# Kernel tuning notes

Measured on AMD Instinct MI355X. Metric: run time of the kernel, lower is better.

## Reference

```python
import jax, jax.numpy as jnp
import numpy as np
from jax import lax

K = 3          # kernel size
PAD = 1        # padding
STRIDE = 1     # stride (output spatial == input spatial)


def conv2d(x, w, b, pad):
    y = lax.conv_general_dilated(x, w, (1, 1), [(pad, pad), (pad, pad)],
                                 dimension_numbers=("NCHW", "OIHW", "NCHW"))
    return y + b[None, :, None, None]


def bilinear_sample(img, y, x):
    """img: [B,C,H,W]; y,x: [B,Ho,Wo] float coords. Zero outside borders (torchvision semantics)."""
    B, C, H, W = img.shape
    flat = img.reshape(B, C, H * W)
    y0 = jnp.floor(y)
    x0 = jnp.floor(x)
    dy = y - y0
    dx = x - x0

    def gather(yc, xc):
        valid = (yc >= 0) & (yc <= H - 1) & (xc >= 0) & (xc <= W - 1)
        yi = jnp.clip(yc, 0, H - 1).astype(jnp.int32)
        xi = jnp.clip(xc, 0, W - 1).astype(jnp.int32)
        idx = (yi * W + xi).reshape(B, -1)                      # [B, Ho*Wo]
        g = jax.vmap(lambda f, i: f[:, i])(flat, idx)            # [B, C, Ho*Wo]
        g = g.reshape(B, C, y.shape[1], y.shape[2])
        return g * valid[:, None, :, :].astype(img.dtype)

    w00 = ((1 - dy) * (1 - dx))[:, None]
    w01 = ((1 - dy) * dx)[:, None]
    w10 = (dy * (1 - dx))[:, None]
    w11 = (dy * dx)[:, None]
    return (gather(y0, x0) * w00 + gather(y0, x0 + 1) * w01 +
            gather(y0 + 1, x0) * w10 + gather(y0 + 1, x0 + 1) * w11)


def deform_conv2d(feat, offset, weight, bias):
    """feat: [B,C,H,W]; offset: [B,2*K*K,Ho,Wo]; weight: [O,C,K,K]; bias: [O]."""
    B, C, H, W = feat.shape
    Ho, Wo = offset.shape[2], offset.shape[3]
    hh = jnp.arange(Ho, dtype=feat.dtype) * STRIDE - PAD   # base y of kernel origin
    ww = jnp.arange(Wo, dtype=feat.dtype) * STRIDE - PAD
    out = jnp.zeros((B, weight.shape[0], Ho, Wo), feat.dtype)
    for i in range(K):
        for j in range(K):
            k = i * K + j
            sy = hh[None, :, None] + i + offset[:, 2 * k]        # [B,Ho,Wo]
            sx = ww[None, None, :] + j + offset[:, 2 * k + 1]
            sampled = bilinear_sample(feat, sy, sx)               # [B,C,Ho,Wo]
            out = out + jnp.einsum("bchw,oc->bohw", sampled, weight[:, :, i, j])
    return out + bias[None, :, None, None]


def setup_inputs() -> dict:
    key = jax.random.key(0)
    ks = jax.random.split(key, 8)
    IN_CH, OUT_CH = 3, 64
    B, H, W = 4, 256, 256
    s1 = 1.0 / np.sqrt(IN_CH * K * K)
    s2 = 1.0 / np.sqrt(OUT_CH * K * K)
    return {
        "x": jax.random.normal(ks[0], (B, IN_CH, H, W), jnp.float32),
        "conv_w": jax.random.normal(ks[1], (OUT_CH, IN_CH, K, K), jnp.float32) * s1,
        "conv_b": jax.random.normal(ks[2], (OUT_CH,), jnp.float32) * s1,
        "offset_w": jax.random.normal(ks[3], (2 * K * K, OUT_CH, K, K), jnp.float32) * 0.01,
        "offset_b": jax.random.normal(ks[4], (2 * K * K,), jnp.float32) * 0.01,
        "deform_w": jax.random.normal(ks[5], (OUT_CH, OUT_CH, K, K), jnp.float32) * s2,
        "deform_b": jax.random.normal(ks[6], (OUT_CH,), jnp.float32) * s2,
    }


def reference(x, conv_w, conv_b, offset_w, offset_b, deform_w, deform_b):
    feat = conv2d(x, conv_w, conv_b, pad=1)                    # [B,64,H,W]
    offset = conv2d(feat, offset_w, offset_b, pad=PAD)          # [B,18,H,W]
    return deform_conv2d(feat, offset, deform_w, deform_b)
```

## Files before the change

### kernel.cpp

```cpp
#include <hip/hip_runtime.h>
#include <hip/hip_fp16.h>

#define FEAT_N (4*64*256*256)
#define OFFS_N (4*18*256*256)
#define WTF_N  (576*64)
#define WT2F_N (576*32)
#define WT1F_N (4*64*8)

typedef __attribute__((ext_vector_type(8))) _Float16 half8;
typedef __attribute__((ext_vector_type(4))) float float4v;
typedef __attribute__((ext_vector_type(4))) unsigned uint4v;

__device__ __forceinline__ unsigned short f2h(float f) {
    union { __half h; unsigned short u; } c; c.h = __float2half_rn(f); return c.u;
}
__device__ __forceinline__ __half2 u2h2(unsigned u) {
    union { unsigned u; __half2 h; } c; c.u = u; return c.h;
}
__device__ __forceinline__ unsigned h22u(__half2 h) {
    union { __half2 h; unsigned u; } c; c.h = h; return c.u;
}

__global__ __launch_bounds__(256) void prep_weights(const float* __restrict__ dw,
                                                    const float* __restrict__ ow,
                                                    const float* __restrict__ cw,
                                                    unsigned short* __restrict__ wtf,
                                                    unsigned short* __restrict__ wt2f,
                                                    unsigned short* __restrict__ wt1f) {
    int idx = blockIdx.x * 256 + threadIdx.x;
    if (idx < WTF_N) {
        int j    = idx & 7;
        int lane = (idx >> 3) & 63;
        int nt   = (idx >> 9) & 3;
        int ks   = idx >> 11;
        int k    = ks * 32 + ((lane >> 4) << 3) + j;
        int tap  = k >> 6;
        int ic   = k & 63;
        int n    = nt * 16 + (lane & 15);
        wtf[idx] = f2h(dw[n * 576 + ic * 9 + tap]);
    }
    int i2 = idx - WTF_N;
    if (i2 >= 0 && i2 < WT2F_N) {
        int j    = i2 & 7;
        int lane = (i2 >> 3) & 63;
        int nt   = (i2 >> 9) & 1;
        int ks   = i2 >> 10;
        int k    = ks * 32 + ((lane >> 4) << 3) + j;
        int tap  = k >> 6;
        int ic   = k & 63;
        int n    = nt * 16 + (lane & 15);
        wt2f[i2] = (n < 18) ? f2h(ow[n * 576 + ic * 9 + tap]) : (unsigned short)0;
    }
    int i3 = idx - WTF_N - WT2F_N;
    if (i3 >= 0 && i3 < WT1F_N) {
        int j    = i3 & 7;
        int lane = (i3 >> 3) & 63;
        int nt   = (i3 >> 9) & 3;
        int n    = nt * 16 + (lane & 15);
        int k    = ((lane >> 4) << 3) + j;
        wt1f[i3] = (k < 27) ? f2h(cw[n * 27 + k]) : (unsigned short)0;
    }
}

__global__ __launch_bounds__(256) void conv1_kernel(const float* __restrict__ x,
                                                    const unsigned short* __restrict__ wt1f,
                                                    const float* __restrict__ cb,
                                                    unsigned short* __restrict__ featp) {
    __shared__ unsigned short xs[10 * 264];
    const int tid  = threadIdx.x;
    const int lane = tid & 63;
    const int wave = tid >> 6;
    const int lm   = lane & 15;
    const int quad = lane >> 4;

    const int bx = blockIdx.x;
    const int b  = bx >> 8;
    const int h  = bx & 255;

#pragma unroll
    for (int r = 0; r < 9; r++) {
        const int ic = r / 3, ti = r % 3;
        const int srow = h - 1 + ti;
        const bool rok = (unsigned)srow < 256u;
        const float* xrow = x + ((b * 3 + ic) << 16) + (srow << 8);
        {
            const int c = tid;
            float v = (rok && (unsigned)(c - 1) < 256u) ? xrow[c - 1] : 0.f;
            xs[r * 264 + c] = f2h(v);
        }
        if (tid < 2) {
            const int c = tid + 256;
            float v = (rok && (unsigned)(c - 1) < 256u) ? xrow[c - 1] : 0.f;
            xs[r * 264 + c] = f2h(v);
        }
    }
    xs[9 * 264 + tid] = 0;
    if (tid < 8) xs[9 * 264 + 256 + tid] = 0;
    __syncthreads();

    int off[8];
#pragma unroll
    for (int j = 0; j < 8; j++) {
        const int k = quad * 8 + j;
        const int row = (k < 27) ? (k / 3) : 9;
        const int tj  = (k < 27) ? (k - row * 3) : 0;
        off[j] = row * 264 + tj;
    }

    half8 bw[4];
#pragma unroll
    for (int nt = 0; nt < 4; nt++)
        bw[nt] = *(const half8*)(wt1f + nt * 512 + lane * 8);
    float bias[4];
#pragma unroll
    for (int nt = 0; nt < 4; nt++) bias[nt] = cb[nt * 16 + lm];

    unsigned short* fpx = featp + ((((size_t)b << 16) + (h << 8)) << 6);

#pragma unroll
    for (int mt = 0; mt < 4; mt++) {
        const int px = wave * 64 + mt * 16 + lm;
        union { half8 v; unsigned u[4]; } af;
#pragma unroll
        for (int jj = 0; jj < 4; jj++) {
            unsigned lo = xs[off[2 * jj]     + px];
            unsigned hi = xs[off[2 * jj + 1] + px];
            af.u[jj] = lo | (hi << 16);
        }
        float4v d[4];
#pragma unroll
        for (int nt = 0; nt < 4; nt++)
            d[nt] = __builtin_amdgcn_mfma_f32_16x16x32_f16(af.v, bw[nt], (float4v)0.f, 0, 0, 0);

        const int pxs = wave * 64 + mt * 16 + quad * 4;
#pragma unroll
        for (int r = 0; r < 4; r++) {
            unsigned short* sp = fpx + (size_t)(pxs + r) * 64 + lm;
#pragma unroll
            for (int nt = 0; nt < 4; nt++)
                sp[nt * 16] = f2h(d[nt][r] + bias[nt]);
        }
    }
}

__global__ __launch_bounds__(256, 2) void fused_kernel(const unsigned short* __restrict__ featp,
                                                       const unsigned short* __restrict__ wt2f,
                                                       const float* __restrict__ ob,
                                                       const unsigned short* __restrict__ wtf,
                                                       const float* __restrict__ db,
                                                       float* __restrict__ out) {
    __shared__ __align__(16) unsigned char ring[4 * 132 * 128];
    __shared__ float offl[4][18 * 33];

    const int tid  = threadIdx.x;
    const int lane = tid & 63;
    const int wave = tid >> 6;
    const int lm   = lane & 15;
    const int quad = lane >> 4;

    const int bx = blockIdx.x;
    const int strip = ((bx & 7) << 8) | (bx >> 3);
    const int wo_base = (strip & 1) << 7;
    const int ho = (strip >> 1) & 255;
    const int b  = strip >> 9;

    const unsigned* fpq = (const unsigned*)featp + ((size_t)b << 21) + quad * 4;
    const int colb = wo_base + wave * 32 + lm;
    float* offw = &offl[wave][0];

    const char* gbase = (const char*)featp + (((size_t)b << 16) << 7);

#define STAGE_ROW(R)                                                             \
    {                                                                            \
        const int rr = (R);                                                      \
        if ((unsigned)rr < 256u) {                                               \
            const char* gsrc = gbase + ((size_t)(rr << 8) << 7);                 \
            const unsigned base = (unsigned)((rr & 3) * 16896);                  \
            for (int c = tid; c < 1056; c += 256) {                              \
                const int xsl = c >> 3;                                          \
                const int col = wo_base - 2 + xsl;                               \
                if ((unsigned)col < 256u) {                                      \
                    uint4v v = *(const uint4v*)(gsrc + (((size_t)col) << 7)      \
                                                + ((c & 7) << 4));               \
                    const unsigned by = base + (unsigned)(c << 4);               \
                    *(uint4v*)(ring + (by ^ ((unsigned)((xsl & 7) << 4)))) = v;  \
                }                                                                \
            }                                                                    \
        }                                                                        \
    }

    STAGE_ROW(ho - 2);
    STAGE_ROW(ho - 1);
    STAGE_ROW(ho);
    STAGE_ROW(ho + 1);

    {
        float4v acc[2][2];
#pragma unroll
        for (int mt = 0; mt < 2; mt++)
#pragma unroll
            for (int nt = 0; nt < 2; nt++) acc[mt][nt] = (float4v)0.f;

        uint4v A[2][2];

#define C2LOAD(KY, KX, DST)                                                      \
    {                                                                            \
        const int row = ho - 1 + (KY);                                           \
        const bool rok = (unsigned)row < 256u;                                   \
        _Pragma("unroll")                                                        \
        for (int mt = 0; mt < 2; mt++) {                                         \
            const int col = colb + mt * 16 + (KX) - 1;                           \
            DST[mt][0] = (uint4v)0;                                              \
            DST[mt][1] = (uint4v)0;                                              \
            if (rok && (unsigned)col < 256u) {                                   \
                const unsigned* p = fpq + (((row << 8) + col) << 5);             \
                DST[mt][0] = *(const uint4v*)p;                                  \
                DST[mt][1] = *(const uint4v*)(p + 16);                           \
            }                                                                    \
        }                                                                        \
    }

        C2LOAD(0, 0, A);

#pragma unroll
        for (int tap = 0; tap < 9; tap++) {
            half8 bfr[2][2];
            const unsigned short* wp = wt2f + (size_t)(tap * 2) * 1024 + lane * 8;
#pragma unroll
            for (int st = 0; st < 2; st++) {
                bfr[st][0] = *(const half8*)(wp + st * 1024);
                bfr[st][1] = *(const half8*)(wp + st * 1024 + 512);
            }
            uint4v N[2][2];
            if (tap < 8) {
                const int tn  = tap + 1;
                const int tky = tn / 3;
                const int tkx = tn - 3 * tky;
                C2LOAD(tky, tkx, N);
            }
#pragma unroll
            for (int mt = 0; mt < 2; mt++) {
                union { half8 v; uint4v u; } f0, f1;
                f0.u = A[mt][0]; f1.u = A[mt][1];
                acc[mt][0] = __builtin_amdgcn_mfma_f32_16x16x32_f16(f0.v, bfr[0][0], acc[mt][0], 0, 0, 0);
                acc[mt][1] = __builtin_amdgcn_mfma_f32_16x16x32_f16(f0.v, bfr[0][1], acc[mt][1], 0, 0, 0);
                acc[mt][0] = __builtin_amdgcn_mfma_f32_16x16x32_f16(f1.v, bfr[1][0], acc[mt][0], 0, 0, 0);
                acc[mt][1] = __builtin_amdgcn_mfma_f32_16x16x32_f16(f1.v, bfr[1][1], acc[mt][1], 0, 0, 0);
            }
            if (tap < 8) {
#pragma unroll
                for (int mt = 0; mt < 2; mt++) {
                    A[mt][0] = N[mt][0];
                    A[mt][1] = N[mt][1];
                }
            }
        }
#undef C2LOAD

#pragma unroll
        for (int nt = 0; nt < 2; nt++) {
            int oc = nt * 16 + lm;
            if (oc < 18) {
                float bv = ob[oc];
#pragma unroll
                for (int mt = 0; mt < 2; mt++) {
#pragma unroll
                    for (int r = 0; r < 4; r++)
                        offw[oc * 33 + mt * 16 + quad * 4 + r] = acc[mt][nt][r] + bv;
                }
            }
        }
    }

    __syncthreads();

    const int wo0 = wo_base + wave * 32 + lm;

    float4v acc[2][4];
#pragma unroll
    for (int mt = 0; mt < 2; mt++)
#pragma unroll
        for (int nt = 0; nt < 4; nt++) acc[mt][nt] = (float4v)0.f;

    union AFU { half8 v; unsigned u[4]; };

#define DOTAP_MT(MT, KY, KX, OY, OX)                                             \
    {                                                                            \
        float sy = (float)(ho - 1 + (KY)) + (OY);                                \
        float sx = (float)(wo0 + (MT) * 16 - 1 + (KX)) + (OX);                   \
        float y0f = floorf(sy), x0f = floorf(sx);                                \
        float dy = sy - y0f, dx = sx - x0f;                                      \
        int y0 = (int)y0f, x0 = (int)x0f;                                        \
        float wy0 = ((unsigned)y0 < 256u) ? (1.f - dy) : 0.f;                    \
        float wy1 = ((unsigned)(y0 + 1) < 256u) ? dy : 0.f;                      \
        float wx0 = ((unsigned)x0 < 256u) ? (1.f - dx) : 0.f;                    \
        float wx1 = ((unsigned)(x0 + 1) < 256u) ? dx : 0.f;                      \
        int yb0 = y0 < 0 ? 0 : (y0 > 255 ? 255 : y0);                            \
        int yb1 = (y0 + 1) < 0 ? 0 : ((y0 + 1) > 255 ? 255 : (y0 + 1));          \
        int xb0 = x0 < 0 ? 0 : (x0 > 255 ? 255 : x0);                            \
        int xb1 = (x0 + 1) < 0 ? 0 : ((x0 + 1) > 255 ? 255 : (x0 + 1));          \
        __half2 W0 = __float2half2_rn(wy0 * wx0);                                \
        __half2 W1 = __float2half2_rn(wy0 * wx1);                                \
        __half2 W2 = __float2half2_rn(wy1 * wx0);                                \
        __half2 W3 = __float2half2_rn(wy1 * wx1);                                \
        uint4v Gg[4][2];                                                         \
        bool inw = (yb0 >= ho - 2 + (KY)) && (yb1 <= ho + (KY) + 1) &&           \
                   (xb0 >= wo_base - 2) && (xb1 <= wo_base + 129);               \
        if (__all(inw)) {                                                        \
            const int xs0 = xb0 - wo_base + 2, xs1 = xb1 - wo_base + 2;          \
            const unsigned m0 = (unsigned)((xs0 & 7) << 4);                      \
            const unsigned m1 = (unsigned)((xs1 & 7) << 4);                      \
            const unsigned r0b = (unsigned)((yb0 & 3) * 16896 + quad * 16);      \
            const unsigned r1b = (unsigned)((yb1 & 3) * 16896 + quad * 16);      \
            const unsigned a00 = r0b + (unsigned)(xs0 << 7);                     \
            const unsigned a01 = r0b + (unsigned)(xs1 << 7);                     \
            const unsigned a10 = r1b + (unsigned)(xs0 << 7);                     \
            const unsigned a11 = r1b + (unsigned)(xs1 << 7);                     \
            Gg[0][0] = *(const uint4v*)(ring + (a00 ^ m0));                      \
            Gg[0][1] = *(const uint4v*)(ring + ((a00 + 64) ^ m0));               \
            Gg[1][0] = *(const uint4v*)(ring + (a01 ^ m1));                      \
            Gg[1][1] = *(const uint4v*)(ring + ((a01 + 64) ^ m1));               \
            Gg[2][0] = *(const uint4v*)(ring + (a10 ^ m0));                      \
            Gg[2][1] = *(const uint4v*)(ring + ((a10 + 64) ^ m0));               \
            Gg[3][0] = *(const uint4v*)(ring + (a11 ^ m1));                      \
            Gg[3][1] = *(const uint4v*)(ring + ((a11 + 64) ^ m1));               \
        } else {                                                                 \
            const unsigned e00 = ((yb0 << 8) + xb0) << 5;                        \
            const unsigned e01 = ((yb0 << 8) + xb1) << 5;                        \
            const unsigned e10 = ((yb1 << 8) + xb0) << 5;                        \
            const unsigned e11 = ((yb1 << 8) + xb1) << 5;                        \
            Gg[0][0] = *(const uint4v*)(fpq + e00);                              \
            Gg[0][1] = *(const uint4v*)(fpq + e00 + 16);                         \
            Gg[1][0] = *(const uint4v*)(fpq + e01);                              \
            Gg[1][1] = *(const uint4v*)(fpq + e01 + 16);                         \
            Gg[2][0] = *(const uint4v*)(fpq + e10);                              \
            Gg[2][1] = *(const uint4v*)(fpq + e10 + 16);                         \
            Gg[3][0] = *(const uint4v*)(fpq + e11);                              \
            Gg[3][1] = *(const uint4v*)(fpq + e11 + 16);                         \
        }                                                                        \
        AFU af[2];                                                               \
        _Pragma("unroll")                                                        \
        for (int st = 0; st < 2; st++) {                                         \
            _Pragma("unroll")                                                    \
            for (int j = 0; j < 4; j++) {                                        \
                __half2 s = __hmul2(W0, u2h2(Gg[0][st][j]));                     \
                s = __hfma2(W1, u2h2(Gg[1][st][j]), s);                          \
                s = __hfma2(W2, u2h2(Gg[2][st][j]), s);                          \
                s = __hfma2(W3, u2h2(Gg[3][st][j]), s);                          \
                af[st].u[j] = h22u(s);                                           \
            }                                                                    \
        }                                                                        \
        _Pragma("unroll")                                                        \
        for (int nt = 0; nt < 4; nt++)                                           \
            acc[MT][nt] = __builtin_amdgcn_mfma_f32_16x16x32_f16(                \
                af[0].v, bfr[0][nt], acc[MT][nt], 0, 0, 0);                      \
        _Pragma("unroll")                                                        \
        for (int nt = 0; nt < 4; nt++)                                           \
            acc[MT][nt] = __builtin_amdgcn_mfma_f32_16x16x32_f16(                \
                af[1].v, bfr[1][nt], acc[MT][nt], 0, 0, 0);                      \
    }

#pragma unroll
    for (int tap = 0; tap < 9; ++tap) {
        const int ky = tap / 3;
        const int kx = tap - 3 * ky;
        if (tap == 3) { __syncthreads(); STAGE_ROW(ho + 2); __syncthreads(); }
        if (tap == 6) { __syncthreads(); STAGE_ROW(ho + 3); __syncthreads(); }

        float oy0 = offw[(2 * tap) * 33 + lm];
        float ox0 = offw[(2 * tap + 1) * 33 + lm];
        float oy1 = offw[(2 * tap) * 33 + lm + 16];
        float ox1 = offw[(2 * tap + 1) * 33 + lm + 16];

        half8 bfr[2][4];
        {
            const unsigned short* wp = wtf + (size_t)tap * 4096 + lane * 8;
#pragma unroll
            for (int nt = 0; nt < 4; nt++) {
                bfr[0][nt] = *(const half8*)(wp + (nt << 9));
                bfr[1][nt] = *(const half8*)(wp + 2048 + (nt << 9));
            }
        }

        DOTAP_MT(0, ky, kx, oy0, ox0);
        DOTAP_MT(1, ky, kx, oy1, ox1);
    }

#pragma unroll
    for (int nt = 0; nt < 4; nt++) {
        int oc = nt * 16 + lm;
        float bv = db[oc];
        float* op = out + (((size_t)(b * 64 + oc)) << 16) + (ho << 8)
                  + wo_base + wave * 32 + quad * 4;
#pragma unroll
        for (int mt = 0; mt < 2; mt++) {
            float4 v = {acc[mt][nt][0] + bv, acc[mt][nt][1] + bv,
                        acc[mt][nt][2] + bv, acc[mt][nt][3] + bv};
            *(float4*)(op + mt * 16) = v;
        }
    }
#undef DOTAP_MT
#undef STAGE_ROW
}

extern "C" void kernel_launch(void* const* d_in, const int* in_sizes, int n_in,
                              void* d_out, int out_size, void* d_ws, size_t ws_size,
                              hipStream_t stream) {
    const float* x  = (const float*)d_in[0];
    const float* cw = (const float*)d_in[1];
    const float* cb = (const float*)d_in[2];
    const float* ow = (const float*)d_in[3];
    const float* ob = (const float*)d_in[4];
    const float* dw = (const float*)d_in[5];
    const float* db = (const float*)d_in[6];
    float* out = (float*)d_out;

    unsigned short* featp = (unsigned short*)d_ws;
    float* offsb = (float*)(featp + FEAT_N);
    unsigned short* wt1f = (unsigned short*)offsb;
    unsigned short* wtf  = (unsigned short*)(offsb + OFFS_N);
    unsigned short* wt2f = wtf + WTF_N;

    prep_weights<<<224, 256, 0, stream>>>(dw, ow, cw, wtf, wt2f, wt1f);
    conv1_kernel<<<1024, 256, 0, stream>>>(x, wt1f, cb, featp);
    fused_kernel<<<2048, 256, 0, stream>>>(featp, wt2f, ob, wtf, db, out);
}
```

Baseline: 213.8 us.

## Split each wave's two M-tiles across separate waves with 512-thread blocks

```diff
diff --git a/kernel.cpp b/kernel.cpp
--- a/kernel.cpp
+++ b/kernel.cpp
@@ -143,7 +143,7 @@
     }
 }
 
-__global__ __launch_bounds__(256, 2) void fused_kernel(const unsigned short* __restrict__ featp,
+__global__ __launch_bounds__(512, 4) void fused_kernel(const unsigned short* __restrict__ featp,
                                                        const unsigned short* __restrict__ wt2f,
                                                        const float* __restrict__ ob,
                                                        const unsigned short* __restrict__ wtf,
@@ -154,7 +154,9 @@
 
     const int tid  = threadIdx.x;
     const int lane = tid & 63;
-    const int wave = tid >> 6;
+    const int wv   = tid >> 6;
+    const int ow   = wv >> 1;
+    const int mtb  = wv & 1;
     const int lm   = lane & 15;
     const int quad = lane >> 4;
 
@@ -165,8 +167,8 @@
     const int b  = strip >> 9;
 
     const unsigned* fpq = (const unsigned*)featp + ((size_t)b << 21) + quad * 4;
-    const int colb = wo_base + wave * 32 + lm;
-    float* offw = &offl[wave][0];
+    const int colb = wo_base + ow * 32 + mtb * 16 + lm;
+    float* offw = &offl[ow][0];
 
     const char* gbase = (const char*)featp + (((size_t)b << 16) << 7);
 
@@ -176,7 +178,7 @@
         if ((unsigned)rr < 256u) {                                               \
             const char* gsrc = gbase + ((size_t)(rr << 8) << 7);                 \
             const unsigned base = (unsigned)((rr & 3) * 16896);                  \
-            for (int c = tid; c < 1056; c += 256) {                              \
+            for (int c = tid; c < 1056; c += 512) {                              \
                 const int xsl = c >> 3;                                          \
                 const int col = wo_base - 2 + xsl;                               \
                 if ((unsigned)col < 256u) {                                      \
@@ -195,28 +197,22 @@
     STAGE_ROW(ho + 1);
 
     {
-        float4v acc[2][2];
-#pragma unroll
-        for (int mt = 0; mt < 2; mt++)
-#pragma unroll
-            for (int nt = 0; nt < 2; nt++) acc[mt][nt] = (float4v)0.f;
-
-        uint4v A[2][2];
+        float4v acc1[2];
+        acc1[0] = (float4v)0.f; acc1[1] = (float4v)0.f;
+
+        uint4v A[2];
 
 #define C2LOAD(KY, KX, DST)                                                      \
     {                                                                            \
         const int row = ho - 1 + (KY);                                           \
         const bool rok = (unsigned)row < 256u;                                   \
-        _Pragma("unroll")                                                        \
-        for (int mt = 0; mt < 2; mt++) {                                         \
-            const int col = colb + mt * 16 + (KX) - 1;                           \
-            DST[mt][0] = (uint4v)0;                                              \
-            DST[mt][1] = (uint4v)0;                                              \
-            if (rok && (unsigned)col < 256u) {                                   \
-                const unsigned* p = fpq + (((row << 8) + col) << 5);             \
-                DST[mt][0] = *(const uint4v*)p;                                  \
-                DST[mt][1] = *(const uint4v*)(p + 16);                           \
-            }                                                                    \
+        const int col = colb + (KX) - 1;                                         \
+        DST[0] = (uint4v)0;                                                      \
+        DST[1] = (uint4v)0;                                                      \
+        if (rok && (unsigned)col < 256u) {                                       \
+            const unsigned* p = fpq + (((row << 8) + col) << 5);                 \
+            DST[0] = *(const uint4v*)p;                                          \
+            DST[1] = *(const uint4v*)(p + 16);                                   \
         }                                                                        \
     }
 
@@ -231,29 +227,22 @@
                 bfr[st][0] = *(const half8*)(wp + st * 1024);
                 bfr[st][1] = *(const half8*)(wp + st * 1024 + 512);
             }
-            uint4v N[2][2];
+            uint4v N[2];
             if (tap < 8) {
                 const int tn  = tap + 1;
                 const int tky = tn / 3;
                 const int tkx = tn - 3 * tky;
                 C2LOAD(tky, tkx, N);
             }
-#pragma unroll
-            for (int mt = 0; mt < 2; mt++) {
+            {
                 union { half8 v; uint4v u; } f0, f1;
-                f0.u = A[mt][0]; f1.u = A[mt][1];
-                acc[mt][0] = __builtin_amdgcn_mfma_f32_16x16x32_f16(f0.v, bfr[0][0], acc[mt][0], 0, 0, 0);
-                acc[mt][1] = __builtin_amdgcn_mfma_f32_16x16x32_f16(f0.v, bfr[0][1], acc[mt][1], 0, 0, 0);
-                acc[mt][0] = __builtin_amdgcn_mfma_f32_16x16x32_f16(f1.v, bfr[1][0], acc[mt][0], 0, 0, 0);
-                acc[mt][1] = __builtin_amdgcn_mfma_f32_16x16x32_f16(f1.v, bfr[1][1], acc[mt][1], 0, 0, 0);
+                f0.u = A[0]; f1.u = A[1];
+                acc1[0] = __builtin_amdgcn_mfma_f32_16x16x32_f16(f0.v, bfr[0][0], acc1[0], 0, 0, 0);
+                acc1[1] = __builtin_amdgcn_mfma_f32_16x16x32_f16(f0.v, bfr[0][1], acc1[1], 0, 0, 0);
+                acc1[0] = __builtin_amdgcn_mfma_f32_16x16x32_f16(f1.v, bfr[1][0], acc1[0], 0, 0, 0);
+                acc1[1] = __builtin_amdgcn_mfma_f32_16x16x32_f16(f1.v, bfr[1][1], acc1[1], 0, 0, 0);
             }
-            if (tap < 8) {
-#pragma unroll
-                for (int mt = 0; mt < 2; mt++) {
-                    A[mt][0] = N[mt][0];
-                    A[mt][1] = N[mt][1];
-                }
-            }
+            if (tap < 8) { A[0] = N[0]; A[1] = N[1]; }
         }
 #undef C2LOAD
 
@@ -263,31 +252,26 @@
             if (oc < 18) {
                 float bv = ob[oc];
 #pragma unroll
-                for (int mt = 0; mt < 2; mt++) {
-#pragma unroll
-                    for (int r = 0; r < 4; r++)
-                        offw[oc * 33 + mt * 16 + quad * 4 + r] = acc[mt][nt][r] + bv;
-                }
+                for (int r = 0; r < 4; r++)
+                    offw[oc * 33 + mtb * 16 + quad * 4 + r] = acc1[nt][r] + bv;
             }
         }
     }
 
     __syncthreads();
 
-    const int wo0 = wo_base + wave * 32 + lm;
-
-    float4v acc[2][4];
-#pragma unroll
-    for (int mt = 0; mt < 2; mt++)
-#pragma unroll
-        for (int nt = 0; nt < 4; nt++) acc[mt][nt] = (float4v)0.f;
+    const int wo0 = wo_base + ow * 32 + mtb * 16 + lm;
+
+    float4v acc[4];
+#pragma unroll
+    for (int nt = 0; nt < 4; nt++) acc[nt] = (float4v)0.f;
 
     union AFU { half8 v; unsigned u[4]; };
 
-#define DOTAP_MT(MT, KY, KX, OY, OX)                                             \
+#define DOTAP(KY, KX, OY, OX)                                                    \
     {                                                                            \
         float sy = (float)(ho - 1 + (KY)) + (OY);                                \
-        float sx = (float)(wo0 + (MT) * 16 - 1 + (KX)) + (OX);                   \
+        float sx = (float)(wo0 - 1 + (KX)) + (OX);                               \
         float y0f = floorf(sy), x0f = floorf(sx);                                \
         float dy = sy - y0f, dx = sx - x0f;                                      \
         int y0 = (int)y0f, x0 = (int)x0f;                                        \
@@ -352,12 +336,12 @@
         }                                                                        \
         _Pragma("unroll")                                                        \
         for (int nt = 0; nt < 4; nt++)                                           \
-            acc[MT][nt] = __builtin_amdgcn_mfma_f32_16x16x32_f16(                \
-                af[0].v, bfr[0][nt], acc[MT][nt], 0, 0, 0);                      \
+            acc[nt] = __builtin_amdgcn_mfma_f32_16x16x32_f16(                    \
+                af[0].v, bfr[0][nt], acc[nt], 0, 0, 0);                          \
         _Pragma("unroll")                                                        \
         for (int nt = 0; nt < 4; nt++)                                           \
-            acc[MT][nt] = __builtin_amdgcn_mfma_f32_16x16x32_f16(                \
-                af[1].v, bfr[1][nt], acc[MT][nt], 0, 0, 0);                      \
+            acc[nt] = __builtin_amdgcn_mfma_f32_16x16x32_f16(                    \
+                af[1].v, bfr[1][nt], acc[nt], 0, 0, 0);                          \
     }
 
 #pragma unroll
@@ -367,10 +351,8 @@
         if (tap == 3) { __syncthreads(); STAGE_ROW(ho + 2); __syncthreads(); }
         if (tap == 6) { __syncthreads(); STAGE_ROW(ho + 3); __syncthreads(); }
 
-        float oy0 = offw[(2 * tap) * 33 + lm];
-        float ox0 = offw[(2 * tap + 1) * 33 + lm];
-        float oy1 = offw[(2 * tap) * 33 + lm + 16];
-        float ox1 = offw[(2 * tap + 1) * 33 + lm + 16];
+        float oy = offw[(2 * tap) * 33 + mtb * 16 + lm];
+        float ox = offw[(2 * tap + 1) * 33 + mtb * 16 + lm];
 
         half8 bfr[2][4];
         {
@@ -382,8 +364,7 @@
             }
         }
 
-        DOTAP_MT(0, ky, kx, oy0, ox0);
-        DOTAP_MT(1, ky, kx, oy1, ox1);
+        DOTAP(ky, kx, oy, ox);
     }
 
 #pragma unroll
@@ -391,15 +372,12 @@
         int oc = nt * 16 + lm;
         float bv = db[oc];
         float* op = out + (((size_t)(b * 64 + oc)) << 16) + (ho << 8)
-                  + wo_base + wave * 32 + quad * 4;
-#pragma unroll
-        for (int mt = 0; mt < 2; mt++) {
-            float4 v = {acc[mt][nt][0] + bv, acc[mt][nt][1] + bv,
-                        acc[mt][nt][2] + bv, acc[mt][nt][3] + bv};
-            *(float4*)(op + mt * 16) = v;
-        }
-    }
-#undef DOTAP_MT
+                  + wo_base + ow * 32 + mtb * 16 + quad * 4;
+        float4 v = {acc[nt][0] + bv, acc[nt][1] + bv,
+                    acc[nt][2] + bv, acc[nt][3] + bv};
+        *(float4*)op = v;
+    }
+#undef DOTAP
 #undef STAGE_ROW
 }
 
@@ -423,5 +401,5 @@
 
     prep_weights<<<224, 256, 0, stream>>>(dw, ow, cw, wtf, wt2f, wt1f);
     conv1_kernel<<<1024, 256, 0, stream>>>(x, wt1f, cb, featp);
-    fused_kernel<<<2048, 256, 0, stream>>>(featp, wt2f, ob, wtf, db, out);
-}
+    fused_kernel<<<2048, 512, 0, stream>>>(featp, wt2f, ob, wtf, db, out);
+}
```

After: 213.2 us. About the same (-0.3%).
